# Kernel optimization log

Hardware: AMD Instinct MI355X
Metric: run time of the kernel (lower is better)

The kernel has to match this reference:

```python
import jax, jax.numpy as jnp
import numpy as np

B, S, D = 8, 2048, 1024
EXPERTS = 8
CAPACITY = 512  # moe_expert_capacity, per batch row along seq axis


def setup_inputs() -> dict:
    key = jax.random.key(0)
    k1, k2, k3 = jax.random.split(key, 3)
    norm_data = jax.random.normal(k1, (B, S, D), dtype=jnp.float32)
    gate_w = jax.random.normal(k2, (EXPERTS, D), dtype=jnp.float32) * 0.02   # nn.Linear weight [E, d]
    expert_w = jax.random.normal(k3, (EXPERTS, D, D), dtype=jnp.float32) * 0.02  # per-expert dense (expert_fn)
    return {"norm_data": norm_data, "gate_w": gate_w, "expert_w": expert_w}


def reference(norm_data, gate_w, expert_w):
    # --- route ---
    router_logits = jnp.einsum('bsd,ed->bse', norm_data, gate_w)            # [B,S,E]
    router_probs = jax.nn.softmax(router_logits.astype(jnp.float32), axis=-1)
    top_expert = jnp.argmax(router_probs, axis=-1)                           # [B,S]
    onehot = jax.nn.one_hot(top_expert, EXPERTS, dtype=jnp.int32)            # [B,S,E]
    token_priority = jnp.cumsum(onehot, axis=-2)                             # cumsum over seq dim
    router_mask = onehot * (token_priority <= CAPACITY).astype(jnp.int32)    # drop over-capacity tokens
    top_prob = jnp.max(router_probs, axis=-1, keepdims=True)                 # [B,S,1]

    # --- dispatch / expert / combine (dropped tokens pass through identity) ---
    next_states = norm_data
    for e in range(EXPERTS):
        out_e = jnp.einsum('bsd,df->bsf', norm_data, expert_w[e])            # [B,S,D]
        keep = (router_mask[:, :, e] > 0)[..., None]                         # [B,S,1]
        next_states = jnp.where(keep, out_e.astype(norm_data.dtype), next_states)

    hidden_states = top_prob.astype(norm_data.dtype) * next_states
    expert_index = jnp.argmax(router_mask, axis=-1)                          # [B,S]
    return (hidden_states, router_logits, expert_index)
```

## Files before the change

kernel.cpp:

```cpp
#include <hip/hip_runtime.h>
#include <hip/hip_bf16.h>
#include <stdint.h>


typedef __attribute__((ext_vector_type(8))) short short8;
typedef __attribute__((ext_vector_type(4))) float f32x4;

#define AS1 __attribute__((address_space(1)))
#define AS3 __attribute__((address_space(3)))

static __device__ __forceinline__ uint32_t f2bf(float f) {
  __hip_bfloat16 h = __float2bfloat16(f);
  return (uint32_t)*reinterpret_cast<unsigned short*>(&h);
}

static __device__ __forceinline__ int resolve_rid(const int* __restrict__ neb,
                                                  const int* __restrict__ slots,
                                                  int e, int g) {
  int acc = 0;
#pragma unroll
  for (int b = 0; b < 8; ++b) {
    int c = neb[e * 8 + b];
    if (g >= acc && g < acc + c) return slots[e * 4096 + b * 512 + (g - acc)];
    acc += c;
  }
  return slots[e * 4096];
}

__global__ __launch_bounds__(256) void k_front(
    const float* __restrict__ x, const float* __restrict__ gw,
    const float* __restrict__ w,
    __hip_bfloat16* __restrict__ xb, __hip_bfloat16* __restrict__ wt,
    float* __restrict__ logits, float* __restrict__ tprob, int* __restrict__ texp) {
  __shared__ __align__(16) float gs[8 * 1024];
  const int tid = threadIdx.x;
  const int bid = blockIdx.x;

  if (bid < 4096) {
    {
      const float4* g4 = reinterpret_cast<const float4*>(gw);
      float4* s4 = reinterpret_cast<float4*>(gs);
#pragma unroll
      for (int i = 0; i < 8; ++i) s4[tid + 256 * i] = g4[tid + 256 * i];
    }
    __syncthreads();
    const int wave = tid >> 6, lane = tid & 63;
    const int t = bid * 4 + wave;
    const float2* x2 = reinterpret_cast<const float2*>(x + (size_t)t * 1024);
    uint32_t* xbu = reinterpret_cast<uint32_t*>(xb + (size_t)t * 1024);
    const float2* g2 = reinterpret_cast<const float2*>(gs);
    float acc[8];
#pragma unroll
    for (int e = 0; e < 8; ++e) acc[e] = 0.f;
#pragma unroll
    for (int kk = 0; kk < 8; ++kk) {
      int p = lane + 64 * kk;
      float2 xv = x2[p];
      xbu[p] = f2bf(xv.x) | (f2bf(xv.y) << 16);
#pragma unroll
      for (int e = 0; e < 8; ++e) {
        float2 g = g2[e * 512 + p];
        acc[e] = fmaf(xv.x, g.x, acc[e]);
        acc[e] = fmaf(xv.y, g.y, acc[e]);
      }
    }
#pragma unroll
    for (int d = 1; d < 64; d <<= 1) {
#pragma unroll
      for (int e = 0; e < 8; ++e) acc[e] += __shfl_xor(acc[e], d, 64);
    }
    if (lane == 0) {
      float m = acc[0];
      int idx = 0;
#pragma unroll
      for (int e = 1; e < 8; ++e)
        if (acc[e] > m) { m = acc[e]; idx = e; }
      float s = 0.f;
#pragma unroll
      for (int e = 0; e < 8; ++e) s += expf(acc[e] - m);
      tprob[t] = 1.0f / s;
      texp[t] = idx;
#pragma unroll
      for (int e = 0; e < 8; ++e) logits[(size_t)t * 8 + e] = acc[e];
    }
  } else {
    const int bx = bid - 4096;
    const int e = bx >> 10;
    const int rem = bx & 1023;
    const int k0 = (rem >> 5) << 5;
    const int n0 = (rem & 31) << 5;
    float (*tile)[33] = reinterpret_cast<float (*)[33]>(gs);
    const int c = tid & 31, r0 = tid >> 5;
    const float* ws = w + (size_t)e * 1024 * 1024;
#pragma unroll
    for (int i = 0; i < 4; ++i) {
      int r = r0 + 8 * i;
      tile[r][c] = ws[(size_t)(k0 + r) * 1024 + n0 + c];
    }
    __syncthreads();
    __hip_bfloat16* wd = wt + (size_t)e * 1024 * 1024;
#pragma unroll
    for (int i = 0; i < 4; ++i) {
      int r = r0 + 8 * i;
      wd[(size_t)(n0 + r) * 1024 + k0 + c] = __float2bfloat16(tile[c][r]);
    }
  }
}

__global__ __launch_bounds__(256) void k_scan(
    const int* __restrict__ texp, int* __restrict__ slots, int* __restrict__ neb,
    int* __restrict__ keep, float* __restrict__ idx_out) {
  const int b = blockIdx.x;
  const int tid = threadIdx.x;
  __shared__ int te_s[2048];
#pragma unroll
  for (int i = 0; i < 8; ++i) te_s[tid + 256 * i] = texp[b * 2048 + tid + 256 * i];
  __syncthreads();

  int myte[8], cnt[8];
#pragma unroll
  for (int e = 0; e < 8; ++e) cnt[e] = 0;
#pragma unroll
  for (int j = 0; j < 8; ++j) {
    int v = te_s[tid * 8 + j];
    myte[j] = v;
#pragma unroll
    for (int e = 0; e < 8; ++e) cnt[e] += (v == e);
  }
  unsigned u0 = (unsigned)cnt[0] | ((unsigned)cnt[1] << 16);
  unsigned u1 = (unsigned)cnt[2] | ((unsigned)cnt[3] << 16);
  unsigned u2 = (unsigned)cnt[4] | ((unsigned)cnt[5] << 16);
  unsigned u3 = (unsigned)cnt[6] | ((unsigned)cnt[7] << 16);
  const int lane = tid & 63, wave = tid >> 6;
#pragma unroll
  for (int d = 1; d < 64; d <<= 1) {
    unsigned v0 = __shfl_up(u0, d, 64);
    unsigned v1 = __shfl_up(u1, d, 64);
    unsigned v2 = __shfl_up(u2, d, 64);
    unsigned v3 = __shfl_up(u3, d, 64);
    if (lane >= d) { u0 += v0; u1 += v1; u2 += v2; u3 += v3; }
  }
  __shared__ unsigned wtot[4][4];
  if (lane == 63) { wtot[wave][0] = u0; wtot[wave][1] = u1; wtot[wave][2] = u2; wtot[wave][3] = u3; }
  __syncthreads();
  unsigned a0 = 0, a1 = 0, a2 = 0, a3 = 0, s0 = 0, s1 = 0, s2 = 0, s3 = 0;
#pragma unroll
  for (int w = 0; w < 4; ++w) {
    unsigned q0 = wtot[w][0], q1 = wtot[w][1], q2 = wtot[w][2], q3 = wtot[w][3];
    if (w < wave) { a0 += q0; a1 += q1; a2 += q2; a3 += q3; }
    s0 += q0; s1 += q1; s2 += q2; s3 += q3;
  }
  u0 += a0; u1 += a1; u2 += a2; u3 += a3;
  int base[8];
  base[0] = (int)(u0 & 0xFFFF) - cnt[0]; base[1] = (int)(u0 >> 16) - cnt[1];
  base[2] = (int)(u1 & 0xFFFF) - cnt[2]; base[3] = (int)(u1 >> 16) - cnt[3];
  base[4] = (int)(u2 & 0xFFFF) - cnt[4]; base[5] = (int)(u2 >> 16) - cnt[5];
  base[6] = (int)(u3 & 0xFFFF) - cnt[6]; base[7] = (int)(u3 >> 16) - cnt[7];
  if (tid == 0) {
    int tt[8] = {(int)(s0 & 0xFFFF), (int)(s0 >> 16), (int)(s1 & 0xFFFF), (int)(s1 >> 16),
                 (int)(s2 & 0xFFFF), (int)(s2 >> 16), (int)(s3 & 0xFFFF), (int)(s3 >> 16)};
#pragma unroll
    for (int e = 0; e < 8; ++e) neb[e * 8 + b] = tt[e] < 512 ? tt[e] : 512;
  }
#pragma unroll
  for (int j = 0; j < 8; ++j) {
    int v = myte[j];
    int rank = 0;
#pragma unroll
    for (int e = 0; e < 8; ++e)
      if (v == e) { base[e] += 1; rank = base[e]; }
    int tok = b * 2048 + tid * 8 + j;
    int kp = rank <= 512;
    keep[tok] = kp;
    idx_out[tok] = kp ? (float)v : 0.0f;
    if (kp) slots[v * 4096 + b * 512 + rank - 1] = tok;
  }
}

__global__ __launch_bounds__(256, 2) void k_gemm(
    const __hip_bfloat16* __restrict__ xb, const __hip_bfloat16* __restrict__ wt,
    const int* __restrict__ neb, const int* __restrict__ slots,
    const float* __restrict__ tprob, float* __restrict__ out) {
  const int bid = blockIdx.x;
  const int tile = (bid & 7) * 64 + (bid >> 3);
  const int e = tile >> 6;
  const int local = tile & 63;
  const int rt = local >> 3;
  const int ct = local & 7;

  extern __shared__ __align__(16) char dynls[];
  __shared__ int rid_s[256];
  __shared__ float tp_s[256];

  const int tid = threadIdx.x;
  const int wave = tid >> 6, lane = tid & 63;
  const int wm = wave >> 1, wn = wave & 1;
  const int frow = lane & 15, qq = lane >> 4;

  int total_cap = 0;
#pragma unroll
  for (int b = 0; b < 8; ++b) total_cap += neb[e * 8 + b];
  int nvalid = total_cap - rt * 256;
  if (nvalid > 256) nvalid = 256;

  if (nvalid > 0) {
    {
      int g = rt * 256 + ((tid < nvalid) ? tid : 0);
      int rid = resolve_rid(neb, slots, e, g);
      rid_s[tid] = rid;
      tp_s[tid] = tprob[rid];
    }
    __syncthreads();

    const __hip_bfloat16* wte = wt + ((size_t)e << 20);
    const __hip_bfloat16* pa[4];
    const __hip_bfloat16* pb[2];
#pragma unroll
    for (int p = 0; p < 4; ++p) {
      int cid = p * 256 + tid;
      int row = cid >> 2, slot = cid & 3;
      int kl = (slot ^ ((row >> 1) & 3)) * 8;
      pa[p] = xb + (size_t)rid_s[row] * 1024 + kl;
    }
#pragma unroll
    for (int p = 0; p < 2; ++p) {
      int cid = p * 256 + tid;
      int row = cid >> 2, slot = cid & 3;
      int kl = (slot ^ ((row >> 1) & 3)) * 8;
      pb[p] = wte + (size_t)(ct * 128 + row) * 1024 + kl;
    }

#define STAGE(kti, bufi)                                                           \
  do {                                                                             \
    char* d_ = dynls + (bufi) * 24576;                                             \
    _Pragma("unroll") for (int p = 0; p < 4; ++p)                                  \
      __builtin_amdgcn_global_load_lds((const AS1 uint32_t*)(pa[p] + (kti) * 32),  \
                                       (AS3 uint32_t*)(d_ + (p * 256 + tid) * 16), 16, 0, 0); \
    _Pragma("unroll") for (int p = 0; p < 2; ++p)                                  \
      __builtin_amdgcn_global_load_lds((const AS1 uint32_t*)(pb[p] + (kti) * 32),  \
                                       (AS3 uint32_t*)(d_ + 16384 + (p * 256 + tid) * 16), 16, 0, 0); \
  } while (0)

    f32x4 acc[8][4];
#pragma unroll
    for (int i = 0; i < 8; ++i)
#pragma unroll
      for (int j = 0; j < 4; ++j) acc[i][j] = 0.f;

    const int sl = qq ^ ((frow >> 1) & 3);
    const int aoffb = (wm * 128 + frow) * 64 + sl * 16;
    const int boffb = (wn * 64 + frow) * 64 + sl * 16;

#define COMPUTE(bufi)                                                              \
  do {                                                                             \
    const char* Ab = dynls + (bufi) * 24576;                                       \
    const char* Bb = Ab + 16384;                                                   \
    short8 a[8], b[4];                                                             \
    _Pragma("unroll") for (int mi = 0; mi < 8; ++mi)                               \
        a[mi] = *reinterpret_cast<const short8*>(Ab + aoffb + mi * 1024);          \
    _Pragma("unroll") for (int ni = 0; ni < 4; ++ni)                               \
        b[ni] = *reinterpret_cast<const short8*>(Bb + boffb + ni * 1024);          \
    __builtin_amdgcn_s_setprio(1);                                                 \
    _Pragma("unroll") for (int mi = 0; mi < 8; ++mi)                               \
        _Pragma("unroll") for (int ni = 0; ni < 4; ++ni)                           \
            acc[mi][ni] = __builtin_amdgcn_mfma_f32_16x16x32_bf16(a[mi], b[ni], acc[mi][ni], 0, 0, 0); \
    __builtin_amdgcn_s_setprio(0);                                                 \
  } while (0)

    STAGE(0, 0);
    STAGE(1, 1);
    for (int t = 0; t < 31; ++t) {
      asm volatile("s_waitcnt vmcnt(6)" ::: "memory");
      __builtin_amdgcn_s_barrier();
      __builtin_amdgcn_sched_barrier(0);
      if (t + 2 < 32) STAGE(t + 2, (t + 2) % 3);
      COMPUTE(t % 3);
    }
    asm volatile("s_waitcnt vmcnt(0)" ::: "memory");
    __builtin_amdgcn_s_barrier();
    __builtin_amdgcn_sched_barrier(0);
    COMPUTE(31 % 3);
#undef COMPUTE
#undef STAGE

    const int colb = ct * 128 + wn * 64 + frow;
    const int rowb = wm * 128 + qq * 4;
#pragma unroll
    for (int mi = 0; mi < 8; ++mi) {
#pragma unroll
      for (int j = 0; j < 4; ++j) {
        int r = rowb + mi * 16 + j;
        if (r < nvalid) {
          size_t ro = (size_t)rid_s[r] * 1024;
          float sc = tp_s[r];
#pragma unroll
          for (int ni = 0; ni < 4; ++ni)
            out[ro + colb + ni * 16] = sc * acc[mi][ni][j];
        }
      }
    }
  }

  int T2 = 0;
  {
#pragma unroll
    for (int ee = 0; ee < 8; ++ee) {
      int s = 0;
#pragma unroll
      for (int b = 0; b < 8; ++b) s += neb[ee * 8 + b];
      int ov = s - 2048; if (ov < 0) ov = 0;
      T2 += ((ov + 31) >> 5) * 8;
    }
  }
  for (int i = bid; i < T2; i += 512) {
    int e2 = 0, loc = i, found = 0;
#pragma unroll
    for (int k = 0; k < 8; ++k) {
      int s = 0;
#pragma unroll
      for (int b = 0; b < 8; ++b) s += neb[k * 8 + b];
      int ov = s - 2048; if (ov < 0) ov = 0;
      int sz = ((ov + 31) >> 5) * 8;
      if (!found) {
        if (loc < sz) { e2 = k; found = 1; } else { loc -= sz; }
      }
    }
    int tot2 = 0;
#pragma unroll
    for (int b = 0; b < 8; ++b) tot2 += neb[e2 * 8 + b];
    const int mc = loc >> 3, ct2 = loc & 7;
    int nv = tot2 - 2048 - mc * 32;
    if (nv > 32) nv = 32;

    __syncthreads();
    if (tid < 32) {
      int g = 2048 + mc * 32 + ((tid < nv) ? tid : 0);
      int rid = resolve_rid(neb, slots, e2, g);
      rid_s[tid] = rid;
      tp_s[tid] = tprob[rid];
    }
    __syncthreads();

    const __hip_bfloat16* wt2 = wt + ((size_t)e2 << 20);
    const __hip_bfloat16* pa0 = xb + (size_t)rid_s[frow] * 1024 + qq * 8;
    const __hip_bfloat16* pa1 = xb + (size_t)rid_s[16 + frow] * 1024 + qq * 8;
    const __hip_bfloat16* pb0 = wt2 + (size_t)(ct2 * 128 + wave * 32 + frow) * 1024 + qq * 8;
    const __hip_bfloat16* pb1 = pb0 + 16 * 1024;
    f32x4 tc00 = 0.f, tc01 = 0.f, tc10 = 0.f, tc11 = 0.f;
#pragma unroll 4
    for (int kk = 0; kk < 32; ++kk) {
      short8 a0 = *reinterpret_cast<const short8*>(pa0);
      short8 a1 = *reinterpret_cast<const short8*>(pa1);
      short8 b0 = *reinterpret_cast<const short8*>(pb0);
      short8 b1 = *reinterpret_cast<const short8*>(pb1);
      tc00 = __builtin_amdgcn_mfma_f32_16x16x32_bf16(a0, b0, tc00, 0, 0, 0);
      tc01 = __builtin_amdgcn_mfma_f32_16x16x32_bf16(a0, b1, tc01, 0, 0, 0);
      tc10 = __builtin_amdgcn_mfma_f32_16x16x32_bf16(a1, b0, tc10, 0, 0, 0);
      tc11 = __builtin_amdgcn_mfma_f32_16x16x32_bf16(a1, b1, tc11, 0, 0, 0);
      pa0 += 32; pa1 += 32; pb0 += 32; pb1 += 32;
    }
    const int colt = ct2 * 128 + wave * 32 + frow;
#pragma unroll
    for (int mi = 0; mi < 2; ++mi) {
#pragma unroll
      for (int j = 0; j < 4; ++j) {
        int r = mi * 16 + qq * 4 + j;
        if (r < nv) {
          float sc = tp_s[r];
          size_t ro = (size_t)rid_s[r] * 1024 + colt;
          out[ro]      = sc * (mi == 0 ? tc00[j] : tc10[j]);
          out[ro + 16] = sc * (mi == 0 ? tc01[j] : tc11[j]);
        }
      }
    }
  }
}

__global__ __launch_bounds__(256) void k_identity(
    const float* __restrict__ x, const float* __restrict__ tprob,
    const int* __restrict__ keep, float* __restrict__ out) {
  const int t0 = blockIdx.x * 8;
  const int tid = threadIdx.x;
#pragma unroll
  for (int j = 0; j < 8; ++j) {
    int t = t0 + j;
    if (!keep[t]) {
      float s = tprob[t];
      const float4* xi = reinterpret_cast<const float4*>(x + (size_t)t * 1024);
      float4* o = reinterpret_cast<float4*>(out + (size_t)t * 1024);
      float4 v = xi[tid];
      o[tid] = make_float4(s * v.x, s * v.y, s * v.z, s * v.w);
    }
  }
}

extern "C" void kernel_launch(void* const* d_in, const int* in_sizes, int n_in,
                              void* d_out, int out_size, void* d_ws, size_t ws_size,
                              hipStream_t stream) {
  const float* x = (const float*)d_in[0];
  const float* gw = (const float*)d_in[1];
  const float* w = (const float*)d_in[2];
  float* out = (float*)d_out;
  float* logits = out + (size_t)16384 * 1024;
  float* idx_out = logits + (size_t)16384 * 8;

  char* ws = (char*)d_ws;
  __hip_bfloat16* xb = (__hip_bfloat16*)(ws);
  __hip_bfloat16* wt = (__hip_bfloat16*)(ws + 33554432);
  float* tprob = (float*)(ws + 50331648);
  int* texp   = (int*)(ws + 50397184);
  int* keep   = (int*)(ws + 50462720);
  int* slots  = (int*)(ws + 50528256);
  int* neb    = (int*)(ws + 50659328);

  hipLaunchKernelGGL(k_front,    dim3(12288), dim3(256), 0, stream, x, gw, w, xb, wt, logits, tprob, texp);
  hipLaunchKernelGGL(k_scan,     dim3(8),     dim3(256), 0, stream, texp, slots, neb, keep, idx_out);
  hipLaunchKernelGGL(k_gemm,     dim3(512),   dim3(256), 73728, stream, xb, wt, neb, slots, tprob, out);
  hipLaunchKernelGGL(k_identity, dim3(2048),  dim3(256), 0, stream, x, tprob, keep, out);
}
```

Measured before the change: 97.59 us.

## Tile expert weights K-blocked, fold identity pass into scan, drop setprio

The transposed bf16 expert weights are now stored K-blocked in 32-wide panels, so each GEMM stage reads a contiguous 8 KB block instead of rows strided by 2 KB. The separate identity kernel is removed. Dropped tokens are instead collected into a shared list inside the scan kernel and scaled there, which saves one launch and the keep array. The MFMA priority hints are also removed. The risk is that only 8 blocks now do the dropped-token copy serially, and the skinny-tail GEMM path has to read with a large stride.

```diff
diff --git a/kernel.cpp b/kernel.cpp
--- a/kernel.cpp
+++ b/kernel.cpp
@@ -98,21 +98,26 @@
       tile[r][c] = ws[(size_t)(k0 + r) * 1024 + n0 + c];
     }
     __syncthreads();
-    __hip_bfloat16* wd = wt + (size_t)e * 1024 * 1024;
+    __hip_bfloat16* wd = wt + (size_t)e * 1024 * 1024 + (size_t)(k0 >> 5) * 32768;
 #pragma unroll
     for (int i = 0; i < 4; ++i) {
       int r = r0 + 8 * i;
-      wd[(size_t)(n0 + r) * 1024 + k0 + c] = __float2bfloat16(tile[c][r]);
+      wd[(size_t)(n0 + r) * 32 + c] = __float2bfloat16(tile[c][r]);
     }
   }
 }
 
 __global__ __launch_bounds__(256) void k_scan(
-    const int* __restrict__ texp, int* __restrict__ slots, int* __restrict__ neb,
-    int* __restrict__ keep, float* __restrict__ idx_out) {
+    const int* __restrict__ texp, const float* __restrict__ x,
+    int* __restrict__ slots, int* __restrict__ neb,
+    float* __restrict__ tprob, float* __restrict__ idx_out,
+    float* __restrict__ out) {
   const int b = blockIdx.x;
   const int tid = threadIdx.x;
   __shared__ int te_s[2048];
+  __shared__ int dlist[2048];
+  __shared__ int ndrop;
+  if (tid == 0) ndrop = 0;
 #pragma unroll
   for (int i = 0; i < 8; ++i) te_s[tid + 256 * i] = texp[b * 2048 + tid + 256 * i];
   __syncthreads();
@@ -171,9 +176,19 @@
       if (v == e) { base[e] += 1; rank = base[e]; }
     int tok = b * 2048 + tid * 8 + j;
     int kp = rank <= 512;
-    keep[tok] = kp;
     idx_out[tok] = kp ? (float)v : 0.0f;
     if (kp) slots[v * 4096 + b * 512 + rank - 1] = tok;
+    else dlist[atomicAdd(&ndrop, 1)] = tok;
+  }
+  __syncthreads();
+  const int nd = ndrop;
+  for (int d = 0; d < nd; ++d) {
+    int tok = dlist[d];
+    float s = tprob[tok];
+    const float4* xi = reinterpret_cast<const float4*>(x + (size_t)tok * 1024);
+    float4* o = reinterpret_cast<float4*>(out + (size_t)tok * 1024);
+    float4 v = xi[tid];
+    o[tid] = make_float4(s * v.x, s * v.y, s * v.z, s * v.w);
   }
 }
 
@@ -227,7 +242,7 @@
       int cid = p * 256 + tid;
       int row = cid >> 2, slot = cid & 3;
       int kl = (slot ^ ((row >> 1) & 3)) * 8;
-      pb[p] = wte + (size_t)(ct * 128 + row) * 1024 + kl;
+      pb[p] = wte + (size_t)ct * 4096 + (size_t)row * 32 + kl;
     }
 
 #define STAGE(kti, bufi)                                                           \
@@ -237,7 +252,7 @@
       __builtin_amdgcn_global_load_lds((const AS1 uint32_t*)(pa[p] + (kti) * 32),  \
                                        (AS3 uint32_t*)(d_ + (p * 256 + tid) * 16), 16, 0, 0); \
     _Pragma("unroll") for (int p = 0; p < 2; ++p)                                  \
-      __builtin_amdgcn_global_load_lds((const AS1 uint32_t*)(pb[p] + (kti) * 32),  \
+      __builtin_amdgcn_global_load_lds((const AS1 uint32_t*)(pb[p] + (size_t)(kti) * 32768), \
                                        (AS3 uint32_t*)(d_ + 16384 + (p * 256 + tid) * 16), 16, 0, 0); \
   } while (0)
 
@@ -260,11 +275,9 @@
         a[mi] = *reinterpret_cast<const short8*>(Ab + aoffb + mi * 1024);          \
     _Pragma("unroll") for (int ni = 0; ni < 4; ++ni)                               \
         b[ni] = *reinterpret_cast<const short8*>(Bb + boffb + ni * 1024);          \
-    __builtin_amdgcn_s_setprio(1);                                                 \
     _Pragma("unroll") for (int mi = 0; mi < 8; ++mi)                               \
         _Pragma("unroll") for (int ni = 0; ni < 4; ++ni)                           \
             acc[mi][ni] = __builtin_amdgcn_mfma_f32_16x16x32_bf16(a[mi], b[ni], acc[mi][ni], 0, 0, 0); \
-    __builtin_amdgcn_s_setprio(0);                                                 \
   } while (0)
 
     STAGE(0, 0);
@@ -344,8 +357,8 @@
     const __hip_bfloat16* wt2 = wt + ((size_t)e2 << 20);
     const __hip_bfloat16* pa0 = xb + (size_t)rid_s[frow] * 1024 + qq * 8;
     const __hip_bfloat16* pa1 = xb + (size_t)rid_s[16 + frow] * 1024 + qq * 8;
-    const __hip_bfloat16* pb0 = wt2 + (size_t)(ct2 * 128 + wave * 32 + frow) * 1024 + qq * 8;
-    const __hip_bfloat16* pb1 = pb0 + 16 * 1024;
+    const __hip_bfloat16* pb0 = wt2 + (size_t)(ct2 * 128 + wave * 32 + frow) * 32 + qq * 8;
+    const __hip_bfloat16* pb1 = pb0 + 16 * 32;
     f32x4 tc00 = 0.f, tc01 = 0.f, tc10 = 0.f, tc11 = 0.f;
 #pragma unroll 4
     for (int kk = 0; kk < 32; ++kk) {
@@ -357,7 +370,7 @@
       tc01 = __builtin_amdgcn_mfma_f32_16x16x32_bf16(a0, b1, tc01, 0, 0, 0);
       tc10 = __builtin_amdgcn_mfma_f32_16x16x32_bf16(a1, b0, tc10, 0, 0, 0);
       tc11 = __builtin_amdgcn_mfma_f32_16x16x32_bf16(a1, b1, tc11, 0, 0, 0);
-      pa0 += 32; pa1 += 32; pb0 += 32; pb1 += 32;
+      pa0 += 32; pa1 += 32; pb0 += 32768; pb1 += 32768;
     }
     const int colt = ct2 * 128 + wave * 32 + frow;
 #pragma unroll
@@ -376,24 +389,6 @@
   }
 }
 
-__global__ __launch_bounds__(256) void k_identity(
-    const float* __restrict__ x, const float* __restrict__ tprob,
-    const int* __restrict__ keep, float* __restrict__ out) {
-  const int t0 = blockIdx.x * 8;
-  const int tid = threadIdx.x;
-#pragma unroll
-  for (int j = 0; j < 8; ++j) {
-    int t = t0 + j;
-    if (!keep[t]) {
-      float s = tprob[t];
-      const float4* xi = reinterpret_cast<const float4*>(x + (size_t)t * 1024);
-      float4* o = reinterpret_cast<float4*>(out + (size_t)t * 1024);
-      float4 v = xi[tid];
-      o[tid] = make_float4(s * v.x, s * v.y, s * v.z, s * v.w);
-    }
-  }
-}
-
 extern "C" void kernel_launch(void* const* d_in, const int* in_sizes, int n_in,
                               void* d_out, int out_size, void* d_ws, size_t ws_size,
                               hipStream_t stream) {
@@ -409,12 +404,10 @@
   __hip_bfloat16* wt = (__hip_bfloat16*)(ws + 33554432);
   float* tprob = (float*)(ws + 50331648);
   int* texp   = (int*)(ws + 50397184);
-  int* keep   = (int*)(ws + 50462720);
-  int* slots  = (int*)(ws + 50528256);
-  int* neb    = (int*)(ws + 50659328);
-
-  hipLaunchKernelGGL(k_front,    dim3(12288), dim3(256), 0, stream, x, gw, w, xb, wt, logits, tprob, texp);
-  hipLaunchKernelGGL(k_scan,     dim3(8),     dim3(256), 0, stream, texp, slots, neb, keep, idx_out);
-  hipLaunchKernelGGL(k_gemm,     dim3(512),   dim3(256), 73728, stream, xb, wt, neb, slots, tprob, out);
-  hipLaunchKernelGGL(k_identity, dim3(2048),  dim3(256), 0, stream, x, tprob, keep, out);
-}
+  int* slots  = (int*)(ws + 50462720);
+  int* neb    = (int*)(ws + 50593792);
+
+  hipLaunchKernelGGL(k_front, dim3(12288), dim3(256), 0, stream, x, gw, w, xb, wt, logits, tprob, texp);
+  hipLaunchKernelGGL(k_scan,  dim3(8),     dim3(256), 0, stream, texp, x, slots, neb, tprob, idx_out, out);
+  hipLaunchKernelGGL(k_gemm,  dim3(512),   dim3(256), 73728, stream, xb, wt, neb, slots, tprob, out);
+}
```

Measured after the change: 92.28 us. -5.4%, faster.
